# Kernel tuning notes

Measured on AMD Instinct MI355X. Metric: run time of the kernel, lower is better.

## Reference

```python
import jax, jax.numpy as jnp
import numpy as np
from jax import lax

NUM_CLASS = 3
PRE_MAX = 4096
POST_MAX = 300
IOU_THR = 0.5
SCORE_THR = 0.05
N_ANCHORS = 321408  # 248*216 BEV grid * 6 anchors per location


def setup_inputs() -> dict:
    key = jax.random.key(0)
    k1, k2, k3, k4, k5, k6 = jax.random.split(key, 6)
    box_preds = jax.random.normal(k1, (1, N_ANCHORS, 7), jnp.float32) * 0.3
    cls_preds = jax.random.normal(k2, (1, N_ANCHORS, NUM_CLASS), jnp.float32)
    dir_preds = jax.random.normal(k3, (1, N_ANCHORS, 2), jnp.float32)
    # anchors [x, y, z, w, l, h, r] at realistic KITTI scale
    xy = jax.random.uniform(k4, (1, N_ANCHORS, 2), jnp.float32, 0.0, 70.0)
    z = jnp.full((1, N_ANCHORS, 1), -1.0, jnp.float32)
    wlh = jax.random.uniform(k5, (1, N_ANCHORS, 3), jnp.float32, 0.5, 4.0)
    r = jax.random.uniform(k6, (1, N_ANCHORS, 1), jnp.float32, -np.pi, np.pi)
    anchors = jnp.concatenate([xy, z, wlh, r], axis=-1)
    return {"box_preds": box_preds, "cls_preds": cls_preds,
            "dir_preds": dir_preds, "anchors": anchors}


def decode_boxes(enc, anchors):
    # SECOND box coder decode, code_size = 7
    xa, ya, za, wa, la, ha, ra = jnp.split(anchors, 7, axis=-1)
    xt, yt, zt, wt, lt, ht, rt = jnp.split(enc, 7, axis=-1)
    za = za + ha * 0.5
    diag = jnp.sqrt(la * la + wa * wa)
    xg = xt * diag + xa
    yg = yt * diag + ya
    zg = zt * ha + za
    lg = jnp.exp(lt) * la
    wg = jnp.exp(wt) * wa
    hg = jnp.exp(ht) * ha
    rg = rt + ra
    zg = zg - hg * 0.5
    return jnp.concatenate([xg, yg, zg, wg, lg, hg, rg], axis=-1)


def standup_boxes(b5):
    # b5: [N,5] = (x, y, w, l, r) -> axis-aligned [xmin, ymin, xmax, ymax]
    centers, dims, ang = b5[:, :2], b5[:, 2:4], b5[:, 4]
    signs = jnp.array([[-1., -1.], [-1., 1.], [1., 1.], [1., -1.]], jnp.float32)
    corners = dims[:, None, :] * 0.5 * signs  # [N,4,2]
    c, s = jnp.cos(ang), jnp.sin(ang)
    rot = jnp.stack([jnp.stack([c, -s], -1), jnp.stack([s, c], -1)], axis=-2)  # [N,2,2]
    corners = jnp.einsum('nkj,nji->nki', corners, rot) + centers[:, None, :]
    return jnp.concatenate([corners.min(axis=1), corners.max(axis=1)], axis=-1)


def pairwise_iou(b):
    # b: [N,4] standup boxes
    area = (b[:, 2] - b[:, 0]) * (b[:, 3] - b[:, 1])
    lt = jnp.maximum(b[:, None, :2], b[None, :, :2])
    rb = jnp.minimum(b[:, None, 2:], b[None, :, 2:])
    wh = jnp.clip(rb - lt, 0.0)
    inter = wh[..., 0] * wh[..., 1]
    return inter / (area[:, None] + area[None, :] - inter + 1e-8)


def greedy_nms(iou, valid):
    n = iou.shape[0]
    def body(keep, i):
        suppressed = jnp.any(keep & (iou[i] > IOU_THR))
        ki = valid[i] & (~suppressed)
        return keep.at[i].set(ki), None
    keep, _ = lax.scan(body, jnp.zeros((n,), bool), jnp.arange(n))
    return keep


def reference(box_preds, cls_preds, dir_preds, anchors):
    boxes = decode_boxes(box_preds[0], anchors[0])          # [N,7]
    scores = jax.nn.sigmoid(cls_preds[0])                   # [N,C]
    dir_labels = jnp.argmax(dir_preds[0], axis=-1)          # [N]
    top_scores = scores.max(axis=-1)
    top_labels = jnp.argmax(scores, axis=-1)
    valid = top_scores >= SCORE_THR
    sc = jnp.where(valid, top_scores, -1.0)
    pre_scores, pre_idx = lax.top_k(sc, PRE_MAX)            # sorted desc
    b_nms = standup_boxes(boxes[pre_idx][:, jnp.array([0, 1, 3, 4, 6])])
    iou = pairwise_iou(b_nms)                               # [PRE,PRE]
    keep = greedy_nms(iou, pre_scores > 0.0)
    kept_sc = jnp.where(keep, pre_scores, -1.0)
    post_sc, post_i = lax.top_k(kept_sc, POST_MAX)
    sel = pre_idx[post_i]                                   # original anchor ids
    v = post_sc > 0.0
    sel_boxes = boxes[sel]
    sel_dir = dir_labels[sel]
    opp = (sel_boxes[:, -1] > 0.0) ^ (sel_dir > 0)
    sel_boxes = sel_boxes.at[:, -1].add(
        jnp.where(opp, jnp.float32(np.pi), jnp.float32(0.0)))
    sel_boxes = jnp.where(v[:, None], sel_boxes, 0.0)
    sel_scores = jnp.where(v, post_sc, 0.0)
    sel_labels = jnp.where(v, top_labels[sel], -1)
    return sel_boxes, sel_scores, sel_labels, v
```

## Files before the change

### kernel.cpp

```cpp
#include <hip/hip_runtime.h>

#pragma clang fp contract(off)

#define N_ANCH 321408
#define NQUAD (N_ANCH / 4)
#define NKB 79
#define KSEL 4096
#define POST 300
#define H1BINS 1024
#define H1BASE 0x3D40u
#define CANDCAP 16384
#define SUPCAP 16
#define WW 256
#define OVFCAP 32
#define ZERO_BYTES (256 + 32768 + 65536 + 16384)
#define ZERO_U4 (ZERO_BYTES / 16)

typedef unsigned int u32;
typedef unsigned long long u64;

__device__ __forceinline__ u32 key_of(float m) {
    float s = 1.0f / (1.0f + expf(-m));
    return (s >= 0.05f) ? __float_as_uint(s) : 0u;
}

__global__ __launch_bounds__(1024) void k_keys(const float4* __restrict__ cls4,
                                               uint4* __restrict__ keys4,
                                               u32* __restrict__ hist_part,
                                               uint4* __restrict__ zbase) {
    __shared__ u32 h0[H1BINS], h1[H1BINS], h2[H1BINS], h3[H1BINS];
    int t = threadIdx.x;
    h0[t] = 0; h1[t] = 0; h2[t] = 0; h3[t] = 0;
    __syncthreads();
    int g = blockIdx.x * 1024 + t;
    if (g < ZERO_U4) zbase[g] = make_uint4(0, 0, 0, 0);
    if (g < NQUAD) {
        float4 a = cls4[g * 3], b = cls4[g * 3 + 1], d = cls4[g * 3 + 2];
        u32 k0 = key_of(fmaxf(a.x, fmaxf(a.y, a.z)));
        u32 k1 = key_of(fmaxf(a.w, fmaxf(b.x, b.y)));
        u32 k2 = key_of(fmaxf(b.z, fmaxf(b.w, d.x)));
        u32 k3 = key_of(fmaxf(d.y, fmaxf(d.z, d.w)));
        keys4[g] = make_uint4(k0, k1, k2, k3);
        u32* hp = ((t & 3) == 0) ? h0 : ((t & 3) == 1) ? h1 : ((t & 3) == 2) ? h2 : h3;
        atomicAdd(&hp[k0 ? ((k0 >> 16) - H1BASE + 1u) : 0u], 1u);
        atomicAdd(&hp[k1 ? ((k1 >> 16) - H1BASE + 1u) : 0u], 1u);
        atomicAdd(&hp[k2 ? ((k2 >> 16) - H1BASE + 1u) : 0u], 1u);
        atomicAdd(&hp[k3 ? ((k3 >> 16) - H1BASE + 1u) : 0u], 1u);
    }
    __syncthreads();
    hist_part[(size_t)t * NKB + blockIdx.x] = h0[t] + h1[t] + h2[t] + h3[t];
}

__global__ __launch_bounds__(1024) void k_scan1(const u32* __restrict__ hist_part,
                                                u32* scal) {
    __shared__ u32 sh[1024];
    int t = threadIdx.x;
    int b = 1023 - t;
    const u32* hp = hist_part + (size_t)b * NKB;
    u32 s = 0;
    #pragma unroll 8
    for (int r = 0; r < NKB; ++r) s += hp[r];
    sh[t] = s;
    __syncthreads();
    for (int off = 1; off < 1024; off <<= 1) {
        u32 x = sh[t];
        u32 y = (t >= off) ? sh[t - off] : 0u;
        __syncthreads();
        sh[t] = x + y;
        __syncthreads();
    }
    u32 incl = sh[t];
    u32 excl = incl - s;
    if (excl < 4096u && incl >= 4096u) {
        scal[8] = (b > 0) ? (u32)(b - 1) + H1BASE : 0u;
    }
    if (t == 1023) scal[9] = incl - s;
}

__global__ __launch_bounds__(256) void k_compact(const uint4* __restrict__ keys4,
                                                 u32* scal, u64* __restrict__ cand) {
    int q = blockIdx.x * 256 + threadIdx.x;
    bool act = q < NQUAD;
    uint4 kv = act ? keys4[q] : make_uint4(0, 0, 0, 0);
    u32 thr16 = scal[8];
    int lane = threadIdx.x & 63;
    u32 i0 = (u32)q * 4u;
    bool p0 = kv.x && (kv.x >> 16) >= thr16;
    bool p1 = kv.y && (kv.y >> 16) >= thr16;
    bool p2 = kv.z && (kv.z >> 16) >= thr16;
    bool p3 = kv.w && (kv.w >> 16) >= thr16;
    u64 b0 = __ballot(p0), b1 = __ballot(p1), b2 = __ballot(p2), b3 = __ballot(p3);
    u32 n0 = (u32)__popcll(b0), n1 = (u32)__popcll(b1), n2 = (u32)__popcll(b2);
    u32 nw = n0 + n1 + n2 + (u32)__popcll(b3);
    u32 base = 0;
    if (lane == 0 && nw) base = atomicAdd(&scal[5], nw);
    base = (u32)__shfl((int)base, 0);
    u64 lt = (lane == 0) ? 0ull : (~0ull >> (64 - lane));
    if (p0) { u32 p = base + (u32)__popcll(b0 & lt);
              if (p < CANDCAP) cand[p] = (((u64)kv.x) << 32) | (u32)(~(i0 + 0)); }
    if (p1) { u32 p = base + n0 + (u32)__popcll(b1 & lt);
              if (p < CANDCAP) cand[p] = (((u64)kv.y) << 32) | (u32)(~(i0 + 1)); }
    if (p2) { u32 p = base + n0 + n1 + (u32)__popcll(b2 & lt);
              if (p < CANDCAP) cand[p] = (((u64)kv.z) << 32) | (u32)(~(i0 + 2)); }
    if (p3) { u32 p = base + n0 + n1 + n2 + (u32)__popcll(b3 & lt);
              if (p < CANDCAP) cand[p] = (((u64)kv.w) << 32) | (u32)(~(i0 + 3)); }
}

__global__ __launch_bounds__(256) void k_rankpart(const u32* __restrict__ scal,
                                                  const u64* __restrict__ cand,
                                                  u32* __restrict__ rank) {
    __shared__ u64 ch[256];
    u32 nc = scal[5]; if (nc > CANDCAP) nc = CANDCAP;
    u32 cb = blockIdx.x * 256u;
    u32 jb = blockIdx.y * 256u;
    if (cb >= nc || jb >= nc) return;
    u32 t = threadIdx.x;
    ch[t] = (jb + t < nc) ? cand[jb + t] : 0ull;
    __syncthreads();
    u32 me = cb + t;
    u64 mine = (me < nc) ? cand[me] : ~0ull;
    u32 r = 0;
    #pragma unroll 8
    for (int j = 0; j < 256; ++j) r += (ch[j] > mine) ? 1u : 0u;
    if (me < nc && r) atomicAdd(&rank[me], r);
}

__device__ __forceinline__ void decode_box(u64 cpack, const float* __restrict__ boxp,
                                           const float* __restrict__ anch, float b[7]) {
    u32 key = (u32)(cpack >> 32);
    u32 idx = ~((u32)(cpack & 0xFFFFFFFFull));
    if (key == 0u) idx = 0u;
    const float* a7 = anch + (size_t)idx * 7;
    const float* t7 = boxp + (size_t)idx * 7;
    float xa = a7[0], ya = a7[1], za = a7[2], wa = a7[3], la = a7[4], ha = a7[5], ra = a7[6];
    float xt = t7[0], yt = t7[1], zt = t7[2], wt = t7[3], lt_ = t7[4], ht = t7[5], rt = t7[6];
    za = za + ha * 0.5f;
    float diag = sqrtf(la * la + wa * wa);
    float xg = xt * diag + xa;
    float yg = yt * diag + ya;
    float zg = zt * ha + za;
    float lg = expf(lt_) * la;
    float wg = expf(wt) * wa;
    float hg = expf(ht) * ha;
    float rg = rt + ra;
    zg = zg - hg * 0.5f;
    b[0] = xg; b[1] = yg; b[2] = zg; b[3] = wg; b[4] = lg; b[5] = hg; b[6] = rg;
}

__device__ __forceinline__ float4 standup_box(const float b[7], float* areao) {
    float xg = b[0], yg = b[1], wg = b[3], lg = b[4], rg = b[6];
    float cc = cosf(rg), ss = sinf(rg);
    float dx = wg * 0.5f, dy = lg * 0.5f;
    const float sxs[4] = {-1.f, -1.f, 1.f, 1.f};
    const float sys[4] = {-1.f, 1.f, 1.f, -1.f};
    float minx = 1e30f, miny = 1e30f, maxx = -1e30f, maxy = -1e30f;
    #pragma unroll
    for (int k = 0; k < 4; ++k) {
        float cx = dx * sxs[k], cy = dy * sys[k];
        float px = cx * cc + cy * ss;
        float py = cx * (-ss) + cy * cc;
        px = px + xg; py = py + yg;
        minx = fminf(minx, px); maxx = fmaxf(maxx, px);
        miny = fminf(miny, py); maxy = fmaxf(maxy, py);
    }
    *areao = (maxx - minx) * (maxy - miny);
    return make_float4(minx, miny, maxx, maxy);
}

__global__ __launch_bounds__(256) void k_scatdec(const u32* __restrict__ scal,
                                                 const u64* __restrict__ cand,
                                                 const u32* __restrict__ rank,
                                                 const float* __restrict__ boxp,
                                                 const float* __restrict__ anch,
                                                 u64* __restrict__ sel2,
                                                 float4* __restrict__ bb,
                                                 float* __restrict__ area) {
    u32 nc = scal[5]; if (nc > CANDCAP) nc = CANDCAP;
    u32 t = blockIdx.x * 256u + threadIdx.x;
    if (t < nc) {
        u32 r = rank[t];
        if (r < (u32)KSEL) {
            u64 cp = cand[t];
            sel2[r] = cp;
            float b[7];
            decode_box(cp, boxp, anch, b);
            float a;
            bb[r] = standup_box(b, &a);
            area[r] = a;
        }
    }
    u32 nvc = scal[9]; if (nvc > (u32)KSEL) nvc = (u32)KSEL;
    if (t >= nvc && t < (u32)KSEL) {
        float b[7];
        decode_box(0ull, boxp, anch, b);
        float a;
        bb[t] = standup_box(b, &a);
        area[t] = a;
    }
}

__global__ __launch_bounds__(256) void k_mask(const float4* __restrict__ bb,
                                              const float* __restrict__ area,
                                              u64* __restrict__ mask,
                                              u32* __restrict__ sup_cnt,
                                              u32* __restrict__ sup_ent) {
    __shared__ float4 ob[256];
    __shared__ float oa[256];
    int t = threadIdx.x;
    int lane = t & 63;
    int w = t >> 6;
    int rb = blockIdx.y;
    int cb = blockIdx.x * 4 + w;
    int i = rb * 64 + lane;
    if (cb < rb) { mask[(size_t)i * 64 + cb] = 0ull; return; }
    int jg0 = cb * 64;
    ob[w * 64 + lane] = bb[jg0 + lane];
    oa[w * 64 + lane] = area[jg0 + lane];
    float4 m4 = bb[i];
    float ma = area[i];
    u64 bits = 0;
    for (int j = 0; j < 64; ++j) {
        int jg = jg0 + j;
        if (jg == i) continue;
        float4 o = ob[w * 64 + j];
        float ltx = fmaxf(m4.x, o.x), lty = fmaxf(m4.y, o.y);
        float rbx = fminf(m4.z, o.z), rby = fminf(m4.w, o.w);
        float wd = fmaxf(rbx - ltx, 0.0f), h = fmaxf(rby - lty, 0.0f);
        float inter = wd * h;
        float iou = inter / (ma + oa[w * 64 + j] - inter + 1e-8f);
        if (iou > 0.5f) bits |= (1ULL << j);
    }
    mask[(size_t)i * 64 + cb] = bits;
    u64 bset = bits;
    while (bset) {
        int j = (int)__builtin_ctzll(bset);
        bset &= bset - 1;
        int jg = jg0 + j;
        if (jg > i) {
            u32 p = atomicAdd(&sup_cnt[i], 1u);
            if (p < SUPCAP) sup_ent[(size_t)i * SUPCAP + p] = (u32)jg;
        }
    }
}

__global__ __launch_bounds__(256, 1) void k_serial(const u64* __restrict__ mask,
                                                   const u32* __restrict__ sup_cnt,
                                                   const u32* __restrict__ sup_ent,
                                                   const u64* __restrict__ sel2,
                                                   const float* __restrict__ boxp,
                                                   const float* __restrict__ anch,
                                                   const float* __restrict__ cls,
                                                   const float* __restrict__ dirp,
                                                   float* __restrict__ out,
                                                   const u32* __restrict__ scal) {
    int t = threadIdx.x;
    int lane = t & 63;
    int wave = t >> 6;
    __shared__ u64 ls_avail[64];
    __shared__ u32 ls_excl[64];
    __shared__ int ls_cand[WW];
    __shared__ u64 ls_m[WW][4];
    __shared__ u64 ls_wv[4];
    __shared__ u64 ls_unc[4];
    __shared__ u32 ls_ovf[OVFCAP];
    __shared__ u32 ls_novf;
    __shared__ u32 ls_keep[POST];

    if (t < 64) {
        u32 nvt = scal[9];
        u32 nv = (nvt < (u32)KSEL) ? nvt : (u32)KSEL;
        int lo = t * 64;
        u64 a;
        if ((int)nv >= lo + 64) a = ~0ull;
        else if ((int)nv <= lo) a = 0ull;
        else a = (((u64)1) << (nv - lo)) - 1ull;
        ls_avail[t] = a;
    }
    __syncthreads();

    int cnt = 0;
    for (;;) {
        ls_m[t][0] = 0; ls_m[t][1] = 0; ls_m[t][2] = 0; ls_m[t][3] = 0;
        ls_cand[t] = -1;
        if (t == 0) ls_novf = 0;
        __syncthreads();
        if (t < 64) {
            u64 avail = ls_avail[t];
            u32 pc = (u32)__popcll(avail);
            u32 pre = pc;
            #pragma unroll
            for (int off = 1; off < 64; off <<= 1) {
                u32 y = __shfl_up(pre, (unsigned)off);
                if (lane >= off) pre += y;
            }
            u32 excl = pre - pc;
            ls_excl[t] = excl;
            if (pc && excl < (u32)WW) {
                u64 a = avail;
                u32 o = excl;
                while (a && o < (u32)WW) {
                    int b = (int)__builtin_ctzll(a);
                    a &= a - 1;
                    ls_cand[o++] = t * 64 + b;
                }
            }
        }
        __syncthreads();
        int cj = ls_cand[t];
        bool valid = cj >= 0;
        {
            u64 wvb = __ballot(valid);
            if (lane == 0) ls_wv[wave] = wvb;
        }
        if (ls_cand[0] < 0) break;
        int cs = valid ? cj : 0;
        const uint4* ep = (const uint4*)(sup_ent + (size_t)cs * SUPCAP);
        uint4 e0 = ep[0], e1 = ep[1], e2 = ep[2], e3 = ep[3];
        u32 scnt = sup_cnt[cs];
        if (!valid) scnt = 0;
        u32 ecap = (scnt < (u32)SUPCAP) ? scnt : (u32)SUPCAP;
        u32 ent[SUPCAP] = {e0.x, e0.y, e0.z, e0.w, e1.x, e1.y, e1.z, e1.w,
                           e2.x, e2.y, e2.z, e2.w, e3.x, e3.y, e3.z, e3.w};
        bool ovf = valid && (scnt > (u32)SUPCAP);
        #pragma unroll
        for (int e = 0; e < SUPCAP; ++e) {
            u32 r = ent[e];
            if ((u32)e < ecap && r < (u32)KSEL) {
                u64 aw = ls_avail[r >> 6];
                if ((aw >> (r & 63)) & 1ull) {
                    u64 below = (r & 63) ? (aw & ((1ull << (r & 63)) - 1ull)) : 0ull;
                    u32 slot = ls_excl[r >> 6] + (u32)__popcll(below);
                    if (slot < (u32)WW)
                        atomicOr(&ls_m[slot][t >> 6], 1ull << (t & 63));
                }
            }
        }
        if (ovf) { u32 p = atomicAdd(&ls_novf, 1u); if (p < OVFCAP) ls_ovf[p] = (u32)t; }
        __syncthreads();
        u32 novf = ls_novf; if (novf > OVFCAP) novf = OVFCAP;
        for (u32 oi = 0; oi < novf; ++oi) {
            int s = (int)ls_ovf[oi];
            int ci = ls_cand[s];
            if (t < 64) {
                u64 w = mask[(size_t)ci * 64 + t] & ls_avail[t];
                while (w) {
                    int b = (int)__builtin_ctzll(w);
                    w &= w - 1;
                    u64 aw = ls_avail[t];
                    u64 below = b ? (aw & ((1ull << b) - 1ull)) : 0ull;
                    u32 slot = ls_excl[t] + (u32)__popcll(below);
                    if (slot < (u32)WW && slot != (u32)s)
                        atomicOr(&ls_m[slot][s >> 6], 1ull << (s & 63));
                }
            }
        }
        __syncthreads();
        u64 my0 = ls_m[t][0], my1 = ls_m[t][1], my2 = ls_m[t][2], my3 = ls_m[t][3];
        bool unc = valid && ((my0 | my1 | my2 | my3) != 0ull);
        {
            u64 ub = __ballot(unc);
            if (lane == 0) ls_unc[wave] = ub;
        }
        __syncthreads();
        u64 wv0 = ls_wv[0], wv1 = ls_wv[1], wv2 = ls_wv[2], wv3 = ls_wv[3];
        u64 u0 = ls_unc[0], u1 = ls_unc[1], u2 = ls_unc[2], u3 = ls_unc[3];
        u64 c0 = wv0 & ~u0, c1 = wv1 & ~u1, c2 = wv2 & ~u2, c3 = wv3 & ~u3;
        #pragma unroll
        for (int blk = 0; blk < 4; ++blk) {
            u64 uw = (blk == 0) ? u0 : (blk == 1) ? u1 : (blk == 2) ? u2 : u3;
            while (uw) {
                int j2 = (int)__builtin_ctzll(uw);
                uw &= uw - 1;
                int j = blk * 64 + j2;
                u64 m0 = ls_m[j][0], m1 = ls_m[j][1], m2 = ls_m[j][2], m3 = ls_m[j][3];
                u64 sup = (m0 & c0) | (m1 & c1) | (m2 & c2) | (m3 & c3);
                if (!sup) {
                    if (blk == 0) c0 |= 1ull << j2;
                    else if (blk == 1) c1 |= 1ull << j2;
                    else if (blk == 2) c2 |= 1ull << j2;
                    else c3 |= 1ull << j2;
                }
            }
        }
        u64 myc = (t < 64) ? c0 : (t < 128) ? c1 : (t < 192) ? c2 : c3;
        bool amC = valid && ((myc >> (t & 63)) & 1ull);
        {
            u32 rk = 0;
            if (wave > 0) rk += (u32)__popcll(c0);
            if (wave > 1) rk += (u32)__popcll(c1);
            if (wave > 2) rk += (u32)__popcll(c2);
            u64 below = (t & 63) ? (myc & ((1ull << (t & 63)) - 1ull)) : 0ull;
            rk += (u32)__popcll(below);
            if (amC && cnt + (int)rk < POST) ls_keep[cnt + rk] = (u32)cj;
        }
        int tot = (int)(__popcll(c0) + __popcll(c1) + __popcll(c2) + __popcll(c3));
        if (cnt + tot >= POST) { cnt = POST; break; }
        cnt += tot;
        if (amC) {
            #pragma unroll
            for (int e = 0; e < SUPCAP; ++e) {
                u32 r = ent[e];
                if ((u32)e < ecap && r < (u32)KSEL)
                    atomicAnd(&ls_avail[r >> 6], ~(1ull << (r & 63)));
            }
            atomicAnd(&ls_avail[cj >> 6], ~(1ull << (cj & 63)));
        }
        for (u32 oi = 0; oi < novf; ++oi) {
            int s = (int)ls_ovf[oi];
            u64 sc = (s < 64) ? c0 : (s < 128) ? c1 : (s < 192) ? c2 : c3;
            if ((sc >> (s & 63)) & 1ull) {
                int ci = ls_cand[s];
                if (t < 64) {
                    u64 w = mask[(size_t)ci * 64 + t];
                    if (w) atomicAnd(&ls_avail[t], ~w);
                }
            }
        }
        __syncthreads();
    }
    __syncthreads();
    u32 m = (u32)(cnt < POST ? cnt : POST);
    float* ob = out;
    float* os = out + POST * 7;
    float* ol = os + POST;
    float* ov = ol + POST;
    for (int o = t; o < POST; o += 256) {
        if (o < (int)m) {
            u32 r = ls_keep[o];
            u64 cp = sel2[r];
            u32 key = (u32)(cp >> 32);
            u32 i = ~((u32)(cp & 0xFFFFFFFFull));
            float b[7];
            decode_box(cp, boxp, anch, b);
            float d0 = dirp[(size_t)i * 2], d1 = dirp[(size_t)i * 2 + 1];
            int dl = (d1 > d0) ? 1 : 0;
            int pos = (b[6] > 0.0f) ? 1 : 0;
            if (pos ^ dl) b[6] = b[6] + 3.14159265358979323846f;
            for (int q = 0; q < 7; ++q) ob[(size_t)o * 7 + q] = b[q];
            os[o] = __uint_as_float(key);
            float s0 = 1.0f / (1.0f + expf(-cls[(size_t)i * 3]));
            float s1 = 1.0f / (1.0f + expf(-cls[(size_t)i * 3 + 1]));
            float s2 = 1.0f / (1.0f + expf(-cls[(size_t)i * 3 + 2]));
            int lab = 0; float best = s0;
            if (s1 > best) { lab = 1; best = s1; }
            if (s2 > best) { lab = 2; }
            ol[o] = (float)lab;
            ov[o] = 1.0f;
        } else {
            for (int q = 0; q < 7; ++q) ob[(size_t)o * 7 + q] = 0.0f;
            os[o] = 0.0f;
            ol[o] = -1.0f;
            ov[o] = 0.0f;
        }
    }
}

extern "C" void kernel_launch(void* const* d_in, const int* in_sizes, int n_in,
                              void* d_out, int out_size, void* d_ws, size_t ws_size,
                              hipStream_t stream) {
    const float* box_preds = (const float*)d_in[0];
    const float* cls_preds = (const float*)d_in[1];
    const float* dir_preds = (const float*)d_in[2];
    const float* anchors   = (const float*)d_in[3];
    float* out = (float*)d_out;

    unsigned char* w = (unsigned char*)d_ws;
    size_t off = 0;
    auto nxt = [&](size_t bytes) -> void* {
        void* p = (void*)(w + off);
        off = (off + bytes + 255) & ~(size_t)255;
        return p;
    };
    u32* scal      = (u32*)nxt(64 * 4);
    u64* sel2      = (u64*)nxt((size_t)KSEL * 8);
    u32* rank      = (u32*)nxt((size_t)CANDCAP * 4);
    u32* sup_cnt   = (u32*)nxt((size_t)KSEL * 4);
    u32* hist_part = (u32*)nxt((size_t)NKB * H1BINS * 4);
    u64* cand      = (u64*)nxt((size_t)CANDCAP * 8);
    u64* mask      = (u64*)nxt((size_t)KSEL * 64 * 8);
    u32* sup_ent   = (u32*)nxt((size_t)KSEL * SUPCAP * 4);
    float4* bb     = (float4*)nxt((size_t)KSEL * 16);
    float* area    = (float*)nxt((size_t)KSEL * 4);
    u32* keys      = (u32*)nxt((size_t)N_ANCH * 4);

    k_keys<<<NKB, 1024, 0, stream>>>((const float4*)cls_preds, (uint4*)keys,
                                     hist_part, (uint4*)scal);
    k_scan1<<<1, 1024, 0, stream>>>(hist_part, scal);
    k_compact<<<(NQUAD + 255) / 256, 256, 0, stream>>>((const uint4*)keys, scal, cand);
    dim3 rg(CANDCAP / 256, CANDCAP / 256);
    k_rankpart<<<rg, 256, 0, stream>>>(scal, cand, rank);
    k_scatdec<<<CANDCAP / 256, 256, 0, stream>>>(scal, cand, rank, box_preds, anchors,
                                                 sel2, bb, area);
    dim3 mg(16, 64);
    k_mask<<<mg, 256, 0, stream>>>(bb, area, mask, sup_cnt, sup_ent);
    k_serial<<<1, 256, 0, stream>>>(mask, sup_cnt, sup_ent, sel2, box_preds, anchors,
                                    cls_preds, dir_preds, out, scal);
}
```

Baseline: 89.02 us.

## Fuse all NMS pipeline stages into one cooperative persistent kernel with grid syncs

Replaces seven separate kernel launches with a single cooperative kernel of 256 blocks that runs every stage in grid-stride loops, using grid.sync() between stages. The goal is to remove per-launch overhead and inter-kernel gaps, which matter because each stage is short. In exchange, every stage runs on a fixed 256-block grid: the key and histogram pass has less parallelism, the scan runs on 256 threads instead of 1024, and each grid barrier has its own cost.

New measurement: 278.5 us. +212.9%, slower.

```diff
diff --git a/kernel.cpp b/kernel.cpp
--- a/kernel.cpp
+++ b/kernel.cpp
@@ -1,10 +1,12 @@
 #include <hip/hip_runtime.h>
+#include <hip/hip_cooperative_groups.h>
 
 #pragma clang fp contract(off)
+
+namespace cg = cooperative_groups;
 
 #define N_ANCH 321408
 #define NQUAD (N_ANCH / 4)
-#define NKB 79
 #define KSEL 4096
 #define POST 300
 #define H1BINS 1024
@@ -13,6 +15,7 @@
 #define SUPCAP 16
 #define WW 256
 #define OVFCAP 32
+#define NBLK 256
 #define ZERO_BYTES (256 + 32768 + 65536 + 16384)
 #define ZERO_U4 (ZERO_BYTES / 16)
 
@@ -22,107 +25,6 @@
 __device__ __forceinline__ u32 key_of(float m) {
     float s = 1.0f / (1.0f + expf(-m));
     return (s >= 0.05f) ? __float_as_uint(s) : 0u;
-}
-
-__global__ __launch_bounds__(1024) void k_keys(const float4* __restrict__ cls4,
-                                               uint4* __restrict__ keys4,
-                                               u32* __restrict__ hist_part,
-                                               uint4* __restrict__ zbase) {
-    __shared__ u32 h0[H1BINS], h1[H1BINS], h2[H1BINS], h3[H1BINS];
-    int t = threadIdx.x;
-    h0[t] = 0; h1[t] = 0; h2[t] = 0; h3[t] = 0;
-    __syncthreads();
-    int g = blockIdx.x * 1024 + t;
-    if (g < ZERO_U4) zbase[g] = make_uint4(0, 0, 0, 0);
-    if (g < NQUAD) {
-        float4 a = cls4[g * 3], b = cls4[g * 3 + 1], d = cls4[g * 3 + 2];
-        u32 k0 = key_of(fmaxf(a.x, fmaxf(a.y, a.z)));
-        u32 k1 = key_of(fmaxf(a.w, fmaxf(b.x, b.y)));
-        u32 k2 = key_of(fmaxf(b.z, fmaxf(b.w, d.x)));
-        u32 k3 = key_of(fmaxf(d.y, fmaxf(d.z, d.w)));
-        keys4[g] = make_uint4(k0, k1, k2, k3);
-        u32* hp = ((t & 3) == 0) ? h0 : ((t & 3) == 1) ? h1 : ((t & 3) == 2) ? h2 : h3;
-        atomicAdd(&hp[k0 ? ((k0 >> 16) - H1BASE + 1u) : 0u], 1u);
-        atomicAdd(&hp[k1 ? ((k1 >> 16) - H1BASE + 1u) : 0u], 1u);
-        atomicAdd(&hp[k2 ? ((k2 >> 16) - H1BASE + 1u) : 0u], 1u);
-        atomicAdd(&hp[k3 ? ((k3 >> 16) - H1BASE + 1u) : 0u], 1u);
-    }
-    __syncthreads();
-    hist_part[(size_t)t * NKB + blockIdx.x] = h0[t] + h1[t] + h2[t] + h3[t];
-}
-
-__global__ __launch_bounds__(1024) void k_scan1(const u32* __restrict__ hist_part,
-                                                u32* scal) {
-    __shared__ u32 sh[1024];
-    int t = threadIdx.x;
-    int b = 1023 - t;
-    const u32* hp = hist_part + (size_t)b * NKB;
-    u32 s = 0;
-    #pragma unroll 8
-    for (int r = 0; r < NKB; ++r) s += hp[r];
-    sh[t] = s;
-    __syncthreads();
-    for (int off = 1; off < 1024; off <<= 1) {
-        u32 x = sh[t];
-        u32 y = (t >= off) ? sh[t - off] : 0u;
-        __syncthreads();
-        sh[t] = x + y;
-        __syncthreads();
-    }
-    u32 incl = sh[t];
-    u32 excl = incl - s;
-    if (excl < 4096u && incl >= 4096u) {
-        scal[8] = (b > 0) ? (u32)(b - 1) + H1BASE : 0u;
-    }
-    if (t == 1023) scal[9] = incl - s;
-}
-
-__global__ __launch_bounds__(256) void k_compact(const uint4* __restrict__ keys4,
-                                                 u32* scal, u64* __restrict__ cand) {
-    int q = blockIdx.x * 256 + threadIdx.x;
-    bool act = q < NQUAD;
-    uint4 kv = act ? keys4[q] : make_uint4(0, 0, 0, 0);
-    u32 thr16 = scal[8];
-    int lane = threadIdx.x & 63;
-    u32 i0 = (u32)q * 4u;
-    bool p0 = kv.x && (kv.x >> 16) >= thr16;
-    bool p1 = kv.y && (kv.y >> 16) >= thr16;
-    bool p2 = kv.z && (kv.z >> 16) >= thr16;
-    bool p3 = kv.w && (kv.w >> 16) >= thr16;
-    u64 b0 = __ballot(p0), b1 = __ballot(p1), b2 = __ballot(p2), b3 = __ballot(p3);
-    u32 n0 = (u32)__popcll(b0), n1 = (u32)__popcll(b1), n2 = (u32)__popcll(b2);
-    u32 nw = n0 + n1 + n2 + (u32)__popcll(b3);
-    u32 base = 0;
-    if (lane == 0 && nw) base = atomicAdd(&scal[5], nw);
-    base = (u32)__shfl((int)base, 0);
-    u64 lt = (lane == 0) ? 0ull : (~0ull >> (64 - lane));
-    if (p0) { u32 p = base + (u32)__popcll(b0 & lt);
-              if (p < CANDCAP) cand[p] = (((u64)kv.x) << 32) | (u32)(~(i0 + 0)); }
-    if (p1) { u32 p = base + n0 + (u32)__popcll(b1 & lt);
-              if (p < CANDCAP) cand[p] = (((u64)kv.y) << 32) | (u32)(~(i0 + 1)); }
-    if (p2) { u32 p = base + n0 + n1 + (u32)__popcll(b2 & lt);
-              if (p < CANDCAP) cand[p] = (((u64)kv.z) << 32) | (u32)(~(i0 + 2)); }
-    if (p3) { u32 p = base + n0 + n1 + n2 + (u32)__popcll(b3 & lt);
-              if (p < CANDCAP) cand[p] = (((u64)kv.w) << 32) | (u32)(~(i0 + 3)); }
-}
-
-__global__ __launch_bounds__(256) void k_rankpart(const u32* __restrict__ scal,
-                                                  const u64* __restrict__ cand,
-                                                  u32* __restrict__ rank) {
-    __shared__ u64 ch[256];
-    u32 nc = scal[5]; if (nc > CANDCAP) nc = CANDCAP;
-    u32 cb = blockIdx.x * 256u;
-    u32 jb = blockIdx.y * 256u;
-    if (cb >= nc || jb >= nc) return;
-    u32 t = threadIdx.x;
-    ch[t] = (jb + t < nc) ? cand[jb + t] : 0ull;
-    __syncthreads();
-    u32 me = cb + t;
-    u64 mine = (me < nc) ? cand[me] : ~0ull;
-    u32 r = 0;
-    #pragma unroll 8
-    for (int j = 0; j < 256; ++j) r += (ch[j] > mine) ? 1u : 0u;
-    if (me < nc && r) atomicAdd(&rank[me], r);
 }
 
 __device__ __forceinline__ void decode_box(u64 cpack, const float* __restrict__ boxp,
@@ -167,95 +69,25 @@
     return make_float4(minx, miny, maxx, maxy);
 }
 
-__global__ __launch_bounds__(256) void k_scatdec(const u32* __restrict__ scal,
-                                                 const u64* __restrict__ cand,
-                                                 const u32* __restrict__ rank,
-                                                 const float* __restrict__ boxp,
-                                                 const float* __restrict__ anch,
-                                                 u64* __restrict__ sel2,
-                                                 float4* __restrict__ bb,
-                                                 float* __restrict__ area) {
-    u32 nc = scal[5]; if (nc > CANDCAP) nc = CANDCAP;
-    u32 t = blockIdx.x * 256u + threadIdx.x;
-    if (t < nc) {
-        u32 r = rank[t];
-        if (r < (u32)KSEL) {
-            u64 cp = cand[t];
-            sel2[r] = cp;
-            float b[7];
-            decode_box(cp, boxp, anch, b);
-            float a;
-            bb[r] = standup_box(b, &a);
-            area[r] = a;
-        }
-    }
-    u32 nvc = scal[9]; if (nvc > (u32)KSEL) nvc = (u32)KSEL;
-    if (t >= nvc && t < (u32)KSEL) {
-        float b[7];
-        decode_box(0ull, boxp, anch, b);
-        float a;
-        bb[t] = standup_box(b, &a);
-        area[t] = a;
-    }
-}
-
-__global__ __launch_bounds__(256) void k_mask(const float4* __restrict__ bb,
-                                              const float* __restrict__ area,
-                                              u64* __restrict__ mask,
-                                              u32* __restrict__ sup_cnt,
-                                              u32* __restrict__ sup_ent) {
+__global__ __launch_bounds__(256, 1) void k_mega(
+        const float4* __restrict__ cls4, const float* __restrict__ boxp,
+        const float* __restrict__ anch, const float* __restrict__ dirp,
+        float* __restrict__ out, uint4* __restrict__ keys4,
+        u32* __restrict__ hist_part, uint4* __restrict__ zbase,
+        u32* __restrict__ scal, u64* __restrict__ sel2, u32* __restrict__ rank,
+        u32* __restrict__ sup_cnt, u64* __restrict__ cand, u64* __restrict__ mask,
+        u32* __restrict__ sup_ent, float4* __restrict__ bb, float* __restrict__ area) {
+    cg::grid_group grid = cg::this_grid();
+    int t = threadIdx.x;
+    int bid = blockIdx.x;
+    int lane = t & 63;
+    int wave = t >> 6;
+
+    __shared__ u32 h0[H1BINS], h1[H1BINS];
+    __shared__ u32 shc[1024], sha[1024], shb[1024];
+    __shared__ u64 ch[256];
     __shared__ float4 ob[256];
     __shared__ float oa[256];
-    int t = threadIdx.x;
-    int lane = t & 63;
-    int w = t >> 6;
-    int rb = blockIdx.y;
-    int cb = blockIdx.x * 4 + w;
-    int i = rb * 64 + lane;
-    if (cb < rb) { mask[(size_t)i * 64 + cb] = 0ull; return; }
-    int jg0 = cb * 64;
-    ob[w * 64 + lane] = bb[jg0 + lane];
-    oa[w * 64 + lane] = area[jg0 + lane];
-    float4 m4 = bb[i];
-    float ma = area[i];
-    u64 bits = 0;
-    for (int j = 0; j < 64; ++j) {
-        int jg = jg0 + j;
-        if (jg == i) continue;
-        float4 o = ob[w * 64 + j];
-        float ltx = fmaxf(m4.x, o.x), lty = fmaxf(m4.y, o.y);
-        float rbx = fminf(m4.z, o.z), rby = fminf(m4.w, o.w);
-        float wd = fmaxf(rbx - ltx, 0.0f), h = fmaxf(rby - lty, 0.0f);
-        float inter = wd * h;
-        float iou = inter / (ma + oa[w * 64 + j] - inter + 1e-8f);
-        if (iou > 0.5f) bits |= (1ULL << j);
-    }
-    mask[(size_t)i * 64 + cb] = bits;
-    u64 bset = bits;
-    while (bset) {
-        int j = (int)__builtin_ctzll(bset);
-        bset &= bset - 1;
-        int jg = jg0 + j;
-        if (jg > i) {
-            u32 p = atomicAdd(&sup_cnt[i], 1u);
-            if (p < SUPCAP) sup_ent[(size_t)i * SUPCAP + p] = (u32)jg;
-        }
-    }
-}
-
-__global__ __launch_bounds__(256, 1) void k_serial(const u64* __restrict__ mask,
-                                                   const u32* __restrict__ sup_cnt,
-                                                   const u32* __restrict__ sup_ent,
-                                                   const u64* __restrict__ sel2,
-                                                   const float* __restrict__ boxp,
-                                                   const float* __restrict__ anch,
-                                                   const float* __restrict__ cls,
-                                                   const float* __restrict__ dirp,
-                                                   float* __restrict__ out,
-                                                   const u32* __restrict__ scal) {
-    int t = threadIdx.x;
-    int lane = t & 63;
-    int wave = t >> 6;
     __shared__ u64 ls_avail[64];
     __shared__ u32 ls_excl[64];
     __shared__ int ls_cand[WW];
@@ -266,6 +98,163 @@
     __shared__ u32 ls_novf;
     __shared__ u32 ls_keep[POST];
 
+    for (int i = t; i < H1BINS; i += 256) { h0[i] = 0; h1[i] = 0; }
+    __syncthreads();
+    for (int g = bid * 256 + t; g < ZERO_U4; g += NBLK * 256)
+        zbase[g] = make_uint4(0, 0, 0, 0);
+    for (int g = bid * 256 + t; g < NQUAD; g += NBLK * 256) {
+        float4 a = cls4[g * 3], b = cls4[g * 3 + 1], d = cls4[g * 3 + 2];
+        u32 k0 = key_of(fmaxf(a.x, fmaxf(a.y, a.z)));
+        u32 k1 = key_of(fmaxf(a.w, fmaxf(b.x, b.y)));
+        u32 k2 = key_of(fmaxf(b.z, fmaxf(b.w, d.x)));
+        u32 k3 = key_of(fmaxf(d.y, fmaxf(d.z, d.w)));
+        keys4[g] = make_uint4(k0, k1, k2, k3);
+        u32* hp = (t & 1) ? h1 : h0;
+        atomicAdd(&hp[k0 ? ((k0 >> 16) - H1BASE + 1u) : 0u], 1u);
+        atomicAdd(&hp[k1 ? ((k1 >> 16) - H1BASE + 1u) : 0u], 1u);
+        atomicAdd(&hp[k2 ? ((k2 >> 16) - H1BASE + 1u) : 0u], 1u);
+        atomicAdd(&hp[k3 ? ((k3 >> 16) - H1BASE + 1u) : 0u], 1u);
+    }
+    __syncthreads();
+    for (int i = t; i < H1BINS; i += 256)
+        hist_part[(size_t)i * NBLK + bid] = h0[i] + h1[i];
+    grid.sync();
+    if (bid == 0) {
+        for (int u = t; u < 1024; u += 256) {
+            int b = 1023 - u;
+            const u32* hp = hist_part + (size_t)b * NBLK;
+            u32 s = 0;
+            #pragma unroll 8
+            for (int r = 0; r < NBLK; ++r) s += hp[r];
+            shc[u] = s; sha[u] = s;
+        }
+        __syncthreads();
+        u32* src = sha; u32* dst = shb;
+        for (int off = 1; off < 1024; off <<= 1) {
+            for (int u = t; u < 1024; u += 256)
+                dst[u] = src[u] + ((u >= off) ? src[u - off] : 0u);
+            __syncthreads();
+            u32* tmp = src; src = dst; dst = tmp;
+        }
+        for (int u = t; u < 1024; u += 256) {
+            u32 incl = src[u];
+            u32 excl = incl - shc[u];
+            int b = 1023 - u;
+            if (excl < 4096u && incl >= 4096u)
+                scal[8] = (b > 0) ? (u32)(b - 1) + H1BASE : 0u;
+        }
+        if (t == 0) scal[9] = src[1023] - shc[1023];
+    }
+    grid.sync();
+    {
+        u32 thr16 = scal[8];
+        int qmax = (NQUAD + NBLK * 256 - 1) / (NBLK * 256) * (NBLK * 256);
+        for (int q = bid * 256 + t; q < qmax; q += NBLK * 256) {
+            bool act = q < NQUAD;
+            uint4 kv = act ? keys4[q] : make_uint4(0, 0, 0, 0);
+            u32 i0 = (u32)q * 4u;
+            bool p0 = kv.x && (kv.x >> 16) >= thr16;
+            bool p1 = kv.y && (kv.y >> 16) >= thr16;
+            bool p2 = kv.z && (kv.z >> 16) >= thr16;
+            bool p3 = kv.w && (kv.w >> 16) >= thr16;
+            u64 b0 = __ballot(p0), b1 = __ballot(p1), b2 = __ballot(p2), b3 = __ballot(p3);
+            u32 n0 = (u32)__popcll(b0), n1 = (u32)__popcll(b1), n2 = (u32)__popcll(b2);
+            u32 nw = n0 + n1 + n2 + (u32)__popcll(b3);
+            u32 base = 0;
+            if (lane == 0 && nw) base = atomicAdd(&scal[5], nw);
+            base = (u32)__shfl((int)base, 0);
+            u64 lt = (lane == 0) ? 0ull : (~0ull >> (64 - lane));
+            if (p0) { u32 p = base + (u32)__popcll(b0 & lt);
+                      if (p < CANDCAP) cand[p] = (((u64)kv.x) << 32) | (u32)(~(i0 + 0)); }
+            if (p1) { u32 p = base + n0 + (u32)__popcll(b1 & lt);
+                      if (p < CANDCAP) cand[p] = (((u64)kv.y) << 32) | (u32)(~(i0 + 1)); }
+            if (p2) { u32 p = base + n0 + n1 + (u32)__popcll(b2 & lt);
+                      if (p < CANDCAP) cand[p] = (((u64)kv.z) << 32) | (u32)(~(i0 + 2)); }
+            if (p3) { u32 p = base + n0 + n1 + n2 + (u32)__popcll(b3 & lt);
+                      if (p < CANDCAP) cand[p] = (((u64)kv.w) << 32) | (u32)(~(i0 + 3)); }
+        }
+    }
+    grid.sync();
+    {
+        u32 nc = scal[5]; if (nc > CANDCAP) nc = CANDCAP;
+        u32 ntile = (nc + 255u) / 256u;
+        for (u32 g = (u32)bid; g < ntile * ntile; g += NBLK) {
+            u32 cb = (g / ntile) * 256u;
+            u32 jb = (g % ntile) * 256u;
+            __syncthreads();
+            ch[t] = (jb + (u32)t < nc) ? cand[jb + t] : 0ull;
+            __syncthreads();
+            u32 me = cb + (u32)t;
+            u64 mine = (me < nc) ? cand[me] : ~0ull;
+            u32 r = 0;
+            #pragma unroll 8
+            for (int j = 0; j < 256; ++j) r += (ch[j] > mine) ? 1u : 0u;
+            if (me < nc && r) atomicAdd(&rank[me], r);
+        }
+    }
+    grid.sync();
+    {
+        u32 nc = scal[5]; if (nc > CANDCAP) nc = CANDCAP;
+        u32 nvc = scal[9]; if (nvc > (u32)KSEL) nvc = (u32)KSEL;
+        for (u32 g = (u32)(bid * 256 + t); g < (u32)CANDCAP; g += NBLK * 256) {
+            if (g < nc) {
+                u32 r = rank[g];
+                if (r < (u32)KSEL) {
+                    u64 cp = cand[g];
+                    sel2[r] = cp;
+                    float b[7];
+                    decode_box(cp, boxp, anch, b);
+                    float a;
+                    bb[r] = standup_box(b, &a);
+                    area[r] = a;
+                }
+            }
+            if (g >= nvc && g < (u32)KSEL) {
+                float b[7];
+                decode_box(0ull, boxp, anch, b);
+                float a;
+                bb[g] = standup_box(b, &a);
+                area[g] = a;
+            }
+        }
+    }
+    grid.sync();
+    for (int g = bid; g < 16 * 64; g += NBLK) {
+        int rb = g >> 4;
+        int cb = (g & 15) * 4 + wave;
+        int i = rb * 64 + lane;
+        if (cb < rb) { mask[(size_t)i * 64 + cb] = 0ull; continue; }
+        int jg0 = cb * 64;
+        ob[wave * 64 + lane] = bb[jg0 + lane];
+        oa[wave * 64 + lane] = area[jg0 + lane];
+        float4 m4 = bb[i];
+        float ma = area[i];
+        u64 bits = 0;
+        for (int j = 0; j < 64; ++j) {
+            int jg = jg0 + j;
+            if (jg == i) continue;
+            float4 o = ob[wave * 64 + j];
+            float ltx = fmaxf(m4.x, o.x), lty = fmaxf(m4.y, o.y);
+            float rbx = fminf(m4.z, o.z), rby = fminf(m4.w, o.w);
+            float wd = fmaxf(rbx - ltx, 0.0f), h = fmaxf(rby - lty, 0.0f);
+            float inter = wd * h;
+            float iou = inter / (ma + oa[wave * 64 + j] - inter + 1e-8f);
+            if (iou > 0.5f) bits |= (1ULL << j);
+        }
+        mask[(size_t)i * 64 + cb] = bits;
+        u64 bset = bits;
+        while (bset) {
+            int j = (int)__builtin_ctzll(bset);
+            bset &= bset - 1;
+            int jg = jg0 + j;
+            if (jg > i) {
+                u32 p = atomicAdd(&sup_cnt[i], 1u);
+                if (p < SUPCAP) sup_ent[(size_t)i * SUPCAP + p] = (u32)jg;
+            }
+        }
+    }
+    grid.sync();
+    if (bid != 0) return;
     if (t < 64) {
         u32 nvt = scal[9];
         u32 nv = (nvt < (u32)KSEL) ? nvt : (u32)KSEL;
@@ -277,7 +266,6 @@
         ls_avail[t] = a;
     }
     __syncthreads();
-
     int cnt = 0;
     for (;;) {
         ls_m[t][0] = 0; ls_m[t][1] = 0; ls_m[t][2] = 0; ls_m[t][3] = 0;
@@ -420,7 +408,8 @@
     }
     __syncthreads();
     u32 m = (u32)(cnt < POST ? cnt : POST);
-    float* ob = out;
+    const float* clsf = (const float*)cls4;
+    float* obp = out;
     float* os = out + POST * 7;
     float* ol = os + POST;
     float* ov = ol + POST;
@@ -436,18 +425,18 @@
             int dl = (d1 > d0) ? 1 : 0;
             int pos = (b[6] > 0.0f) ? 1 : 0;
             if (pos ^ dl) b[6] = b[6] + 3.14159265358979323846f;
-            for (int q = 0; q < 7; ++q) ob[(size_t)o * 7 + q] = b[q];
+            for (int q = 0; q < 7; ++q) obp[(size_t)o * 7 + q] = b[q];
             os[o] = __uint_as_float(key);
-            float s0 = 1.0f / (1.0f + expf(-cls[(size_t)i * 3]));
-            float s1 = 1.0f / (1.0f + expf(-cls[(size_t)i * 3 + 1]));
-            float s2 = 1.0f / (1.0f + expf(-cls[(size_t)i * 3 + 2]));
-            int lab = 0; float best = s0;
-            if (s1 > best) { lab = 1; best = s1; }
-            if (s2 > best) { lab = 2; }
+            float t0 = 1.0f / (1.0f + expf(-clsf[(size_t)i * 3]));
+            float t1 = 1.0f / (1.0f + expf(-clsf[(size_t)i * 3 + 1]));
+            float t2 = 1.0f / (1.0f + expf(-clsf[(size_t)i * 3 + 2]));
+            int lab = 0; float best = t0;
+            if (t1 > best) { lab = 1; best = t1; }
+            if (t2 > best) { lab = 2; }
             ol[o] = (float)lab;
             ov[o] = 1.0f;
         } else {
-            for (int q = 0; q < 7; ++q) ob[(size_t)o * 7 + q] = 0.0f;
+            for (int q = 0; q < 7; ++q) obp[(size_t)o * 7 + q] = 0.0f;
             os[o] = 0.0f;
             ol[o] = -1.0f;
             ov[o] = 0.0f;
@@ -475,7 +464,7 @@
     u64* sel2      = (u64*)nxt((size_t)KSEL * 8);
     u32* rank      = (u32*)nxt((size_t)CANDCAP * 4);
     u32* sup_cnt   = (u32*)nxt((size_t)KSEL * 4);
-    u32* hist_part = (u32*)nxt((size_t)NKB * H1BINS * 4);
+    u32* hist_part = (u32*)nxt((size_t)NBLK * H1BINS * 4);
     u64* cand      = (u64*)nxt((size_t)CANDCAP * 8);
     u64* mask      = (u64*)nxt((size_t)KSEL * 64 * 8);
     u32* sup_ent   = (u32*)nxt((size_t)KSEL * SUPCAP * 4);
@@ -483,16 +472,13 @@
     float* area    = (float*)nxt((size_t)KSEL * 4);
     u32* keys      = (u32*)nxt((size_t)N_ANCH * 4);
 
-    k_keys<<<NKB, 1024, 0, stream>>>((const float4*)cls_preds, (uint4*)keys,
-                                     hist_part, (uint4*)scal);
-    k_scan1<<<1, 1024, 0, stream>>>(hist_part, scal);
-    k_compact<<<(NQUAD + 255) / 256, 256, 0, stream>>>((const uint4*)keys, scal, cand);
-    dim3 rg(CANDCAP / 256, CANDCAP / 256);
-    k_rankpart<<<rg, 256, 0, stream>>>(scal, cand, rank);
-    k_scatdec<<<CANDCAP / 256, 256, 0, stream>>>(scal, cand, rank, box_preds, anchors,
-                                                 sel2, bb, area);
-    dim3 mg(16, 64);
-    k_mask<<<mg, 256, 0, stream>>>(bb, area, mask, sup_cnt, sup_ent);
-    k_serial<<<1, 256, 0, stream>>>(mask, sup_cnt, sup_ent, sel2, box_preds, anchors,
-                                    cls_preds, dir_preds, out, scal);
+    const float4* cls4 = (const float4*)cls_preds;
+    uint4* keys4 = (uint4*)keys;
+    uint4* zbase = (uint4*)scal;
+    void* args[] = {(void*)&cls4, (void*)&box_preds, (void*)&anchors, (void*)&dir_preds,
+                    (void*)&out, (void*)&keys4, (void*)&hist_part, (void*)&zbase,
+                    (void*)&scal, (void*)&sel2, (void*)&rank, (void*)&sup_cnt,
+                    (void*)&cand, (void*)&mask, (void*)&sup_ent, (void*)&bb,
+                    (void*)&area};
+    (void)hipLaunchCooperativeKernel((void*)k_mega, dim3(NBLK), dim3(256), args, 0, stream);
 }
```
